# Kernel optimization log

Measured on AMD Instinct MI355X. Metric: run time of the kernel, lower is better.

Reference implementation:

```python
import jax, jax.numpy as jnp
import numpy as np

N = 100000   # nodes
E = 1600000  # edges
F = 64       # num_features
H = 64       # hidden_units
C = 10       # num_classes
G = 1000     # graphs in batch
BN_EPS = 1e-5


def setup_inputs() -> dict:
    key = jax.random.key(0)
    ks = jax.random.split(key, 32)
    inp = {
        "x": jax.random.normal(ks[0], (N, F), dtype=jnp.float32),
        "edge_index": jax.random.randint(ks[1], (2, E), 0, N, dtype=jnp.int64),
        "batch": jnp.sort(jax.random.randint(ks[2], (N,), 0, G, dtype=jnp.int64)),
    }
    i = 3
    def w(shape, scale):
        nonlocal i
        a = jax.random.normal(ks[i], shape, dtype=jnp.float32) * scale
        i += 1
        return a
    for l, din in [(0, F), (1, H)]:
        inp[f"c{l}_w1"] = w((din, H), 1.0 / np.sqrt(din))
        inp[f"c{l}_b1"] = jnp.zeros((H,), jnp.float32)
        inp[f"c{l}_g1"] = jnp.ones((H,), jnp.float32)
        inp[f"c{l}_be1"] = jnp.zeros((H,), jnp.float32)
        inp[f"c{l}_w2"] = w((H, H), 1.0 / np.sqrt(H))
        inp[f"c{l}_b2"] = jnp.zeros((H,), jnp.float32)
        inp[f"bn{l}_g"] = jnp.ones((H,), jnp.float32)
        inp[f"bn{l}_b"] = jnp.zeros((H,), jnp.float32)
    for l, din in [(0, F), (1, H), (2, H)]:
        inp[f"l{l}_w"] = w((din, C), 1.0 / np.sqrt(din))
        inp[f"l{l}_b"] = jnp.zeros((C,), jnp.float32)
    return inp


def _bn(h, g, b):
    # BatchNorm1d in training mode: batch statistics over node axis
    m = jnp.mean(h, axis=0)
    v = jnp.var(h, axis=0)
    return g * (h - m) * jax.lax.rsqrt(v + BN_EPS) + b


def _gin_conv(h, src, dst, w1, b1, g1, be1, w2, b2):
    # scatter-add neighbor aggregation: out[dst] += h[src]; eps = 0
    agg = jax.ops.segment_sum(h[src], dst, num_segments=N)
    z = h + agg                      # (1 + eps) * x + sum_j x_j
    z = jax.nn.relu(_bn(z @ w1 + b1, g1, be1))
    return z @ w2 + b2


def reference(x, edge_index, batch,
              c0_w1, c0_b1, c0_g1, c0_be1, c0_w2, c0_b2, bn0_g, bn0_b,
              c1_w1, c1_b1, c1_g1, c1_be1, c1_w2, c1_b2, bn1_g, bn1_b,
              l0_w, l0_b, l1_w, l1_b, l2_w, l2_b):
    src, dst = edge_index[0], edge_index[1]
    h0 = x
    h1 = jax.nn.relu(_bn(_gin_conv(h0, src, dst, c0_w1, c0_b1, c0_g1, c0_be1, c0_w2, c0_b2), bn0_g, bn0_b))
    h2 = jax.nn.relu(_bn(_gin_conv(h1, src, dst, c1_w1, c1_b1, c1_g1, c1_be1, c1_w2, c1_b2), bn1_g, bn1_b))
    # jumping-knowledge readout: per-layer global_add_pool -> Linear -> sum (dropout=0)
    out = jnp.zeros((G, C), dtype=x.dtype)
    for h, w, b in [(h0, l0_w, l0_b), (h1, l1_w, l1_b), (h2, l2_w, l2_b)]:
        pooled = jax.ops.segment_sum(h, batch, num_segments=G)
        out = out + pooled @ w + b
    return out
```

## Files before the change

### kernel.cpp

```cpp
#include <hip/hip_runtime.h>
#include <hip/hip_bf16.h>

#define BN_EPS 1e-5f
#define NBMAX 512
#define CHUNK 4096
#define CAPC  6144

typedef __hip_bfloat16 bf16;
typedef __attribute__((ext_vector_type(8))) short short8;
typedef __attribute__((ext_vector_type(4))) float f32x4;

__device__ __forceinline__ float b2f(bf16 v) { return __bfloat162float(v); }
__device__ __forceinline__ bf16 f2b(float v) { return __float2bfloat16(v); }
__device__ __forceinline__ float bl(unsigned u) { return __uint_as_float(u << 16); }
__device__ __forceinline__ float bh(unsigned u) { return __uint_as_float(u & 0xffff0000u); }
__device__ __forceinline__ unsigned pack2(float x, float y) {
    union { bf16 b[2]; unsigned u; } p;
    p.b[0] = f2b(x); p.b[1] = f2b(y);
    return p.u;
}
__device__ __forceinline__ float bs2f(short s) {
    return __uint_as_float(((unsigned)(unsigned short)s) << 16);
}
__device__ __forceinline__ short f2bs(float v) {
    bf16 b = f2b(v);
    return *reinterpret_cast<short*>(&b);
}

__global__ __launch_bounds__(256) void initcast_k(
    const float* __restrict__ in, bf16* __restrict__ out, int total4,
    int* __restrict__ btot, int nbp1)
{
    if (blockIdx.x == 0) {
        for (int i = threadIdx.x; i < nbp1; i += 256) btot[i] = 0;
    }
    int i = blockIdx.x * 256 + threadIdx.x;
    if (i >= total4) return;
    float4 v = ((const float4*)in)[i];
    union { ushort4 u; bf16 b[4]; } p;
    p.b[0] = f2b(v.x); p.b[1] = f2b(v.y); p.b[2] = f2b(v.z); p.b[3] = f2b(v.w);
    ((ushort4*)out)[i] = p.u;
}


__global__ __launch_bounds__(256) void bincount_k(
    const int* __restrict__ dst, int* __restrict__ btot, int E, int NB)
{
    __shared__ int h[NBMAX];
    for (int i = threadIdx.x; i < NB; i += 256) h[i] = 0;
    __syncthreads();
    const int base = blockIdx.x * CHUNK;
    const int lim = min(CHUNK, E - base);
    for (int i = threadIdx.x; i < lim; i += 256)
        atomicAdd(&h[dst[base + i] >> 8], 1);
    __syncthreads();
    for (int i = threadIdx.x; i < NB; i += 256)
        if (h[i]) atomicAdd(&btot[i], h[i]);
}

__global__ __launch_bounds__(256) void bucketscan_k(
    const int* __restrict__ btot, int* __restrict__ bbase,
    int* __restrict__ bcur, int* __restrict__ rowptr, int NB, int N, int E)
{
    __shared__ int s[256];
    const int t = threadIdx.x;
    int v0 = (2 * t     < NB) ? btot[2 * t]     : 0;
    int v1 = (2 * t + 1 < NB) ? btot[2 * t + 1] : 0;
    s[t] = v0 + v1;
    __syncthreads();
    for (int off = 1; off < 256; off <<= 1) {
        int a = (t >= off) ? s[t - off] : 0;
        __syncthreads();
        s[t] += a;
        __syncthreads();
    }
    int excl = s[t] - (v0 + v1);
    if (2 * t < NB)     { bbase[2 * t] = excl;          bcur[2 * t] = excl; }
    if (2 * t + 1 < NB) { bbase[2 * t + 1] = excl + v0; bcur[2 * t + 1] = excl + v0; }
    if (t == 0) { bbase[NB] = E; rowptr[N] = E; }
}

__global__ __launch_bounds__(256) void binscatter_k(
    const int* __restrict__ src, const int* __restrict__ dst,
    int* __restrict__ bcur, int* __restrict__ tmp, int E, int NB)
{
    __shared__ int hist[NBMAX];
    __shared__ int loff[NBMAX];
    __shared__ int gb[NBMAX];
    __shared__ int lcur[NBMAX];
    __shared__ int staged[CHUNK];
    __shared__ unsigned short sb[CHUNK];
    __shared__ int ssc[256];
    const int t = threadIdx.x;
    for (int i = t; i < NB; i += 256) { hist[i] = 0; lcur[i] = 0; }
    __syncthreads();
    const int base = blockIdx.x * CHUNK;
    const int lim = min(CHUNK, E - base);
    int myb[16], myw[16];
    int cnt = 0;
    for (int i = t; i < lim; i += 256) {
        int d = dst[base + i];
        int s_ = src[base + i];
        int b = d >> 8;
        myb[cnt] = b;
        myw[cnt] = (s_ << 8) | (d & 255);
        cnt++;
        atomicAdd(&hist[b], 1);
    }
    __syncthreads();
    int v0 = (2 * t     < NB) ? hist[2 * t]     : 0;
    int v1 = (2 * t + 1 < NB) ? hist[2 * t + 1] : 0;
    ssc[t] = v0 + v1;
    __syncthreads();
    for (int off = 1; off < 256; off <<= 1) {
        int a = (t >= off) ? ssc[t - off] : 0;
        __syncthreads();
        ssc[t] += a;
        __syncthreads();
    }
    int excl = ssc[t] - (v0 + v1);
    if (2 * t < NB)     loff[2 * t] = excl;
    if (2 * t + 1 < NB) loff[2 * t + 1] = excl + v0;
    __syncthreads();
    for (int b = t; b < NB; b += 256)
        if (hist[b] > 0) gb[b] = atomicAdd(&bcur[b], hist[b]);
    for (int i = 0; i < cnt; i++) {
        int b = myb[i];
        int p = loff[b] + atomicAdd(&lcur[b], 1);
        staged[p] = myw[i];
        sb[p] = (unsigned short)b;
    }
    __syncthreads();
    for (int i = t; i < lim; i += 256) {
        int b = sb[i];
        tmp[gb[b] + (i - loff[b])] = staged[i];
    }
}

__global__ __launch_bounds__(256) void csr_k(
    const int* __restrict__ bbase, const int* __restrict__ tmp,
    int* __restrict__ rowptr, int* __restrict__ adj, int N)
{
    __shared__ int hist[256], pfx[256], cur[256], ssc[256];
    __shared__ int sadj[CAPC];
    const int b = blockIdx.x, t = threadIdx.x;
    const int lo = bbase[b], hi = bbase[b + 1];
    const int cnt = hi - lo;
    hist[t] = 0; cur[t] = 0;
    __syncthreads();
    for (int i = t; i < cnt; i += 256)
        atomicAdd(&hist[tmp[lo + i] & 255], 1);
    __syncthreads();
    int v = hist[t];
    ssc[t] = v;
    __syncthreads();
    for (int off = 1; off < 256; off <<= 1) {
        int a = (t >= off) ? ssc[t - off] : 0;
        __syncthreads();
        ssc[t] += a;
        __syncthreads();
    }
    pfx[t] = ssc[t] - v;
    const int node = b * 256 + t;
    if (node < N) rowptr[node] = lo + pfx[t];
    __syncthreads();
    if (cnt <= CAPC) {
        for (int i = t; i < cnt; i += 256) {
            int w = tmp[lo + i];
            int d = w & 255;
            int p = pfx[d] + atomicAdd(&cur[d], 1);
            sadj[p] = w >> 8;
        }
        __syncthreads();
        for (int i = t; i < cnt; i += 256) adj[lo + i] = sadj[i];
    } else {
        for (int i = t; i < cnt; i += 256) {
            int w = tmp[lo + i];
            int d = w & 255;
            int p = pfx[d] + atomicAdd(&cur[d], 1);
            adj[lo + p] = w >> 8;
        }
    }
}

template<int AFFINE>
__global__ __launch_bounds__(256) void aggregate_k(
    const bf16* __restrict__ h, const int* __restrict__ rowptr,
    const int* __restrict__ adj, bf16* __restrict__ z, int N,
    const float* __restrict__ sc, const float* __restrict__ sh)
{
    const int lane = threadIdx.x & 31;
    const int n = blockIdx.x * 8 + (threadIdx.x >> 5);
    float sc0 = 0.f, sc1 = 0.f, sh0 = 0.f, sh1 = 0.f;
    if (AFFINE) {
        const int f0 = lane * 2;
        sc0 = sc[f0]; sc1 = sc[f0 + 1];
        sh0 = sh[f0]; sh1 = sh[f0 + 1];
    }
    if (n >= N) return;
    const unsigned* hp = (const unsigned*)h;
    const int b = rowptr[n], e = rowptr[n + 1];

    unsigned u = hp[(size_t)n * 32 + lane];
    float a0 = bl(u), a1 = bh(u);
    if (AFFINE) {
        a0 = fmaxf(fmaf(a0, sc0, sh0), 0.f);
        a1 = fmaxf(fmaf(a1, sc1, sh1), 0.f);
    }
    float s0 = a0, s1 = a1;

    int i = b;
    for (; i + 16 <= e; i += 16) {
        int m[16];
        #pragma unroll
        for (int k = 0; k < 16; k++) m[k] = adj[i + k];
        unsigned w[16];
        #pragma unroll
        for (int k = 0; k < 16; k++) w[k] = hp[(size_t)m[k] * 32 + lane];
        #pragma unroll
        for (int k = 0; k < 16; k++) {
            float p0 = bl(w[k]), p1 = bh(w[k]);
            if (AFFINE) {
                p0 = fmaxf(fmaf(p0, sc0, sh0), 0.f);
                p1 = fmaxf(fmaf(p1, sc1, sh1), 0.f);
            }
            s0 += p0; s1 += p1;
        }
    }
    for (; i + 4 <= e; i += 4) {
        int m[4];
        #pragma unroll
        for (int k = 0; k < 4; k++) m[k] = adj[i + k];
        #pragma unroll
        for (int k = 0; k < 4; k++) {
            unsigned w = hp[(size_t)m[k] * 32 + lane];
            float p0 = bl(w), p1 = bh(w);
            if (AFFINE) {
                p0 = fmaxf(fmaf(p0, sc0, sh0), 0.f);
                p1 = fmaxf(fmaf(p1, sc1, sh1), 0.f);
            }
            s0 += p0; s1 += p1;
        }
    }
    for (; i < e; i++) {
        unsigned w = hp[(size_t)adj[i] * 32 + lane];
        float p0 = bl(w), p1 = bh(w);
        if (AFFINE) {
            p0 = fmaxf(fmaf(p0, sc0, sh0), 0.f);
            p1 = fmaxf(fmaf(p1, sc1, sh1), 0.f);
        }
        s0 += p0; s1 += p1;
    }
    ((unsigned*)z)[(size_t)n * 32 + lane] = pack2(s0, s1);
}

template<int MODE>
__global__ __launch_bounds__(256) void gemm64_k(
    const bf16* __restrict__ A,
    const float* __restrict__ scin, const float* __restrict__ shin,
    const float* __restrict__ W, const float* __restrict__ bias,
    bf16* __restrict__ out, float* __restrict__ pstat, int nrows)
{
    __shared__ bf16 sWt[64][72];
    __shared__ float sSc[64], sSh[64], sB[64];
    __shared__ float sredS[64][17], sredQ[64][17];
    const int tid = threadIdx.x;

    if (tid < 64) {
        sB[tid] = bias[tid];
        if (MODE == 1) { sSc[tid] = scin[tid]; sSh[tid] = shin[tid]; }
    }
    for (int i = tid; i < 4096; i += 256) {
        int k = i >> 6, n = i & 63;
        sWt[n][k] = f2b(W[i]);
    }
    __syncthreads();

    const int wave = tid >> 6, lane = tid & 63;
    const int quad = lane >> 4, l16 = lane & 15;
    const int row0 = blockIdx.x * 128 + wave * 32;

    short8 a[2][2];
    #pragma unroll
    for (int rt = 0; rt < 2; rt++) {
        int r = row0 + rt * 16 + l16;
        int rr = min(r, nrows - 1);
        const bf16* arow = A + (size_t)rr * 64;
        a[rt][0] = *(const short8*)(arow + quad * 8);
        a[rt][1] = *(const short8*)(arow + 32 + quad * 8);
        if (MODE == 1) {
            #pragma unroll
            for (int j = 0; j < 8; j++) {
                int f0 = quad * 8 + j;
                a[rt][0][j] = f2bs(fmaxf(fmaf(bs2f(a[rt][0][j]), sSc[f0], sSh[f0]), 0.f));
                int f1 = 32 + f0;
                a[rt][1][j] = f2bs(fmaxf(fmaf(bs2f(a[rt][1][j]), sSc[f1], sSh[f1]), 0.f));
            }
        }
    }

    float psS[4], psQ[4];
    #pragma unroll
    for (int t = 0; t < 4; t++) { psS[t] = 0.f; psQ[t] = 0.f; }

    #pragma unroll
    for (int t = 0; t < 4; t++) {
        const int n = t * 16 + l16;
        short8 b0 = *(const short8*)&sWt[n][quad * 8];
        short8 b1 = *(const short8*)&sWt[n][32 + quad * 8];
        const float bn_ = sB[n];
        #pragma unroll
        for (int rt = 0; rt < 2; rt++) {
            f32x4 acc = {0.f, 0.f, 0.f, 0.f};
            acc = __builtin_amdgcn_mfma_f32_16x16x32_bf16(a[rt][0], b0, acc, 0, 0, 0);
            acc = __builtin_amdgcn_mfma_f32_16x16x32_bf16(a[rt][1], b1, acc, 0, 0, 0);
            #pragma unroll
            for (int reg = 0; reg < 4; reg++) {
                int gr = row0 + rt * 16 + quad * 4 + reg;
                if (gr < nrows) {
                    float v = acc[reg] + bn_;
                    out[(size_t)gr * 64 + n] = f2b(v);
                    psS[t] += v;
                    psQ[t] = fmaf(v, v, psQ[t]);
                }
            }
        }
    }

    #pragma unroll
    for (int t = 0; t < 4; t++) {
        sredS[t * 16 + l16][wave * 4 + quad] = psS[t];
        sredQ[t * 16 + l16][wave * 4 + quad] = psQ[t];
    }
    __syncthreads();
    if (tid < 128) {
        const int c = tid & 63;
        const float* p = (tid < 64) ? &sredS[c][0] : &sredQ[c][0];
        float s = 0.f;
        #pragma unroll
        for (int i = 0; i < 16; i++) s += p[i];
        pstat[(size_t)blockIdx.x * 128 + (tid < 64 ? c : 64 + c)] = s;
    }
}

__global__ __launch_bounds__(256) void bn_reduce_k(
    const float* __restrict__ pstat, int nblk,
    const float* __restrict__ g, const float* __restrict__ be, float invN,
    float* __restrict__ sc, float* __restrict__ sh)
{
    const int f = blockIdx.x;
    const int t = threadIdx.x;
    float S = 0.f, Q = 0.f;
    for (int b = t; b < nblk; b += 256) {
        S += pstat[(size_t)b * 128 + f];
        Q += pstat[(size_t)b * 128 + 64 + f];
    }
    __shared__ float rs[256], rq[256];
    rs[t] = S; rq[t] = Q;
    __syncthreads();
    for (int off = 128; off > 0; off >>= 1) {
        if (t < off) { rs[t] += rs[t + off]; rq[t] += rq[t + off]; }
        __syncthreads();
    }
    if (t == 0) {
        float m = rs[0] * invN;
        float v = rq[0] * invN - m * m;
        float s = g[f] * rsqrtf(v + BN_EPS);
        sc[f] = s;
        sh[f] = be[f] - m * s;
    }
}

__global__ __launch_bounds__(256) void pool_readout_k(
    const bf16* __restrict__ xb, const bf16* __restrict__ z0,
    const bf16* __restrict__ z1, const int* __restrict__ batch,
    const float* __restrict__ scA, const float* __restrict__ shA,
    const float* __restrict__ scB, const float* __restrict__ shB,
    const float* __restrict__ w0, const float* __restrict__ b0,
    const float* __restrict__ w1, const float* __restrict__ b1,
    const float* __restrict__ w2, const float* __restrict__ b2,
    float* __restrict__ out, int Nn)
{
    const int g = blockIdx.x;
    int lo = 0, hi = Nn;
    while (lo < hi) { int mid = (lo + hi) >> 1; if (batch[mid] < g) lo = mid + 1; else hi = mid; }
    const int start = lo;
    hi = Nn;
    while (lo < hi) { int mid = (lo + hi) >> 1; if (batch[mid] <= g) lo = mid + 1; else hi = mid; }
    const int end = lo;

    const int f = threadIdx.x & 63;
    const int w = threadIdx.x >> 6;
    const float sA = scA[f], tA = shA[f];
    const float sB = scB[f], tB = shB[f];

    float s0 = 0.f, s1 = 0.f, s2 = 0.f;
    for (int i = start + w; i < end; i += 4) {
        s0 += b2f(xb[(size_t)i * 64 + f]);
        s1 += fmaxf(fmaf(b2f(z0[(size_t)i * 64 + f]), sA, tA), 0.f);
        s2 += fmaxf(fmaf(b2f(z1[(size_t)i * 64 + f]), sB, tB), 0.f);
    }
    __shared__ float p[3][4][64];
    p[0][w][f] = s0; p[1][w][f] = s1; p[2][w][f] = s2;
    __syncthreads();
    if (threadIdx.x < 10) {
        const int c = threadIdx.x;
        float acc = b0[c] + b1[c] + b2[c];
        for (int k = 0; k < 64; k++) {
            float q0 = p[0][0][k] + p[0][1][k] + p[0][2][k] + p[0][3][k];
            float q1 = p[1][0][k] + p[1][1][k] + p[1][2][k] + p[1][3][k];
            float q2 = p[2][0][k] + p[2][1][k] + p[2][2][k] + p[2][3][k];
            acc = fmaf(q0, w0[k * 10 + c], acc);
            acc = fmaf(q1, w1[k * 10 + c], acc);
            acc = fmaf(q2, w2[k * 10 + c], acc);
        }
        out[(size_t)g * 10 + c] = acc;
    }
}

extern "C" void kernel_launch(void* const* d_in, const int* in_sizes, int n_in,
                              void* d_out, int out_size, void* d_ws, size_t ws_size,
                              hipStream_t stream)
{
    const float* x     = (const float*)d_in[0];
    const int*   edge  = (const int*)d_in[1];
    const int*   batch = (const int*)d_in[2];
    const int N = in_sizes[0] / 64;
    const int E = in_sizes[1] / 2;
    const int G = out_size / 10;
    const int* src = edge;
    const int* dst = edge + E;
    const int NB = (N + 255) / 256;

    const float* c_w1[2]  = {(const float*)d_in[3],  (const float*)d_in[11]};
    const float* c_b1[2]  = {(const float*)d_in[4],  (const float*)d_in[12]};
    const float* c_g1[2]  = {(const float*)d_in[5],  (const float*)d_in[13]};
    const float* c_be1[2] = {(const float*)d_in[6],  (const float*)d_in[14]};
    const float* c_w2[2]  = {(const float*)d_in[7],  (const float*)d_in[15]};
    const float* c_b2[2]  = {(const float*)d_in[8],  (const float*)d_in[16]};
    const float* bn_g[2]  = {(const float*)d_in[9],  (const float*)d_in[17]};
    const float* bn_b[2]  = {(const float*)d_in[10], (const float*)d_in[18]};
    const float* lw[3]    = {(const float*)d_in[19], (const float*)d_in[21], (const float*)d_in[23]};
    const float* lb[3]    = {(const float*)d_in[20], (const float*)d_in[22], (const float*)d_in[24]};

    float* out = (float*)d_out;
    const size_t nh = (size_t)N * 64;
    const int PG = (N + 127) / 128;

    bf16*  zb    = (bf16*)d_ws;
    bf16*  wb    = zb + nh;
    bf16*  xb    = wb + nh;
    float* scsh  = (float*)(xb + nh);
    float* pstat = scsh + 512;
    int*   rowptr   = (int*)(pstat + (size_t)PG * 128);
    int*   adj      = rowptr + N + 1;
    int*   tmp      = adj + E;
    int*   btot     = tmp + E;
    int*   bbase    = btot + NB + 1;
    int*   bcur     = bbase + NB + 1;

    float* sc0 = scsh;       float* sh0 = scsh + 64;
    float* scA = scsh + 128; float* shA = scsh + 192;
    float* sc2 = scsh + 256; float* sh2 = scsh + 320;
    float* scB = scsh + 384; float* shB = scsh + 448;

    const float invN = 1.0f / (float)N;
    const int binGrid  = (E + CHUNK - 1) / CHUNK;
    const int aggGrid  = (N + 7) / 8;
    const int ewGrid   = (int)((nh / 4 + 255) / 256);

    initcast_k<<<ewGrid, 256, 0, stream>>>(x, xb, (int)(nh / 4), btot, NB + 1);
    bincount_k<<<binGrid, 256, 0, stream>>>(dst, btot, E, NB);
    bucketscan_k<<<1, 256, 0, stream>>>(btot, bbase, bcur, rowptr, NB, N, E);
    binscatter_k<<<binGrid, 256, 0, stream>>>(src, dst, bcur, tmp, E, NB);
    csr_k<<<NB, 256, 0, stream>>>(bbase, tmp, rowptr, adj, N);

    aggregate_k<0><<<aggGrid, 256, 0, stream>>>(xb, rowptr, adj, zb, N, nullptr, nullptr);
    gemm64_k<0><<<PG, 256, 0, stream>>>(zb, nullptr, nullptr,
                                        c_w1[0], c_b1[0], zb, pstat, N);
    bn_reduce_k<<<64, 256, 0, stream>>>(pstat, PG, c_g1[0], c_be1[0], invN, sc0, sh0);
    gemm64_k<1><<<PG, 256, 0, stream>>>(zb, sc0, sh0,
                                        c_w2[0], c_b2[0], zb, pstat, N);
    bn_reduce_k<<<64, 256, 0, stream>>>(pstat, PG, bn_g[0], bn_b[0], invN, scA, shA);

    aggregate_k<1><<<aggGrid, 256, 0, stream>>>(zb, rowptr, adj, wb, N, scA, shA);
    gemm64_k<0><<<PG, 256, 0, stream>>>(wb, nullptr, nullptr,
                                        c_w1[1], c_b1[1], wb, pstat, N);
    bn_reduce_k<<<64, 256, 0, stream>>>(pstat, PG, c_g1[1], c_be1[1], invN, sc2, sh2);
    gemm64_k<1><<<PG, 256, 0, stream>>>(wb, sc2, sh2,
                                        c_w2[1], c_b2[1], wb, pstat, N);
    bn_reduce_k<<<64, 256, 0, stream>>>(pstat, PG, bn_g[1], bn_b[1], invN, scB, shB);

    pool_readout_k<<<G, 256, 0, stream>>>(xb, zb, wb, batch,
                                          scA, shA, scB, shB,
                                          lw[0], lb[0], lw[1], lb[1], lw[2], lb[2],
                                          out, N);
}
```

Measured before the change: 327.4 us.

## Degree-sort nodes within buckets and aggregate with 16 lanes per node

```diff
diff --git a/kernel.cpp b/kernel.cpp
--- a/kernel.cpp
+++ b/kernel.cpp
@@ -139,14 +139,16 @@
 
 __global__ __launch_bounds__(256) void csr_k(
     const int* __restrict__ bbase, const int* __restrict__ tmp,
-    int* __restrict__ rowptr, int* __restrict__ adj, int N)
+    int* __restrict__ rowptr, int* __restrict__ adj,
+    int* __restrict__ perm, int N)
 {
     __shared__ int hist[256], pfx[256], cur[256], ssc[256];
+    __shared__ int dh[256], dcur[256];
     __shared__ int sadj[CAPC];
     const int b = blockIdx.x, t = threadIdx.x;
     const int lo = bbase[b], hi = bbase[b + 1];
     const int cnt = hi - lo;
-    hist[t] = 0; cur[t] = 0;
+    hist[t] = 0; cur[t] = 0; dh[t] = 0; dcur[t] = 0;
     __syncthreads();
     for (int i = t; i < cnt; i += 256)
         atomicAdd(&hist[tmp[lo + i] & 255], 1);
@@ -163,7 +165,25 @@
     pfx[t] = ssc[t] - v;
     const int node = b * 256 + t;
     if (node < N) rowptr[node] = lo + pfx[t];
-    __syncthreads();
+
+    int deg = min(v, 255);
+    atomicAdd(&dh[deg], 1);
+    __syncthreads();
+    int dv = dh[t];
+    ssc[t] = dv;
+    __syncthreads();
+    for (int off = 1; off < 256; off <<= 1) {
+        int a = (t >= off) ? ssc[t - off] : 0;
+        __syncthreads();
+        ssc[t] += a;
+        __syncthreads();
+    }
+    dh[t] = ssc[t] - dv;
+    __syncthreads();
+    int rank = dh[deg] + atomicAdd(&dcur[deg], 1);
+    perm[b * 256 + rank] = node;
+    __syncthreads();
+
     if (cnt <= CAPC) {
         for (int i = t; i < cnt; i += 256) {
             int w = tmp[lo + i];
@@ -186,72 +206,68 @@
 template<int AFFINE>
 __global__ __launch_bounds__(256) void aggregate_k(
     const bf16* __restrict__ h, const int* __restrict__ rowptr,
-    const int* __restrict__ adj, bf16* __restrict__ z, int N,
+    const int* __restrict__ adj, const int* __restrict__ perm,
+    bf16* __restrict__ z, int N,
     const float* __restrict__ sc, const float* __restrict__ sh)
 {
-    const int lane = threadIdx.x & 31;
-    const int n = blockIdx.x * 8 + (threadIdx.x >> 5);
-    float sc0 = 0.f, sc1 = 0.f, sh0 = 0.f, sh1 = 0.f;
+    const int lane = threadIdx.x & 15;
+    const int slot = blockIdx.x * 16 + (threadIdx.x >> 4);
+    float4 vsc, vsh;
     if (AFFINE) {
-        const int f0 = lane * 2;
-        sc0 = sc[f0]; sc1 = sc[f0 + 1];
-        sh0 = sh[f0]; sh1 = sh[f0 + 1];
-    }
+        vsc = ((const float4*)sc)[lane];
+        vsh = ((const float4*)sh)[lane];
+    }
+    const int n = perm[slot];
     if (n >= N) return;
-    const unsigned* hp = (const unsigned*)h;
+    const uint2* hp = (const uint2*)h;
     const int b = rowptr[n], e = rowptr[n + 1];
 
-    unsigned u = hp[(size_t)n * 32 + lane];
-    float a0 = bl(u), a1 = bh(u);
+    uint2 u = hp[(size_t)n * 16 + lane];
+    float a0 = bl(u.x), a1 = bh(u.x), a2 = bl(u.y), a3 = bh(u.y);
     if (AFFINE) {
-        a0 = fmaxf(fmaf(a0, sc0, sh0), 0.f);
-        a1 = fmaxf(fmaf(a1, sc1, sh1), 0.f);
-    }
-    float s0 = a0, s1 = a1;
+        a0 = fmaxf(fmaf(a0, vsc.x, vsh.x), 0.f);
+        a1 = fmaxf(fmaf(a1, vsc.y, vsh.y), 0.f);
+        a2 = fmaxf(fmaf(a2, vsc.z, vsh.z), 0.f);
+        a3 = fmaxf(fmaf(a3, vsc.w, vsh.w), 0.f);
+    }
+    float s0 = a0, s1 = a1, s2 = a2, s3 = a3;
 
     int i = b;
-    for (; i + 16 <= e; i += 16) {
-        int m[16];
+    for (; i + 8 <= e; i += 8) {
+        int m[8];
         #pragma unroll
-        for (int k = 0; k < 16; k++) m[k] = adj[i + k];
-        unsigned w[16];
+        for (int k = 0; k < 8; k++) m[k] = adj[i + k];
+        uint2 w[8];
         #pragma unroll
-        for (int k = 0; k < 16; k++) w[k] = hp[(size_t)m[k] * 32 + lane];
+        for (int k = 0; k < 8; k++) w[k] = hp[(size_t)m[k] * 16 + lane];
         #pragma unroll
-        for (int k = 0; k < 16; k++) {
-            float p0 = bl(w[k]), p1 = bh(w[k]);
+        for (int k = 0; k < 8; k++) {
+            float p0 = bl(w[k].x), p1 = bh(w[k].x);
+            float p2 = bl(w[k].y), p3 = bh(w[k].y);
             if (AFFINE) {
-                p0 = fmaxf(fmaf(p0, sc0, sh0), 0.f);
-                p1 = fmaxf(fmaf(p1, sc1, sh1), 0.f);
+                p0 = fmaxf(fmaf(p0, vsc.x, vsh.x), 0.f);
+                p1 = fmaxf(fmaf(p1, vsc.y, vsh.y), 0.f);
+                p2 = fmaxf(fmaf(p2, vsc.z, vsh.z), 0.f);
+                p3 = fmaxf(fmaf(p3, vsc.w, vsh.w), 0.f);
             }
-            s0 += p0; s1 += p1;
-        }
-    }
-    for (; i + 4 <= e; i += 4) {
-        int m[4];
-        #pragma unroll
-        for (int k = 0; k < 4; k++) m[k] = adj[i + k];
-        #pragma unroll
-        for (int k = 0; k < 4; k++) {
-            unsigned w = hp[(size_t)m[k] * 32 + lane];
-            float p0 = bl(w), p1 = bh(w);
-            if (AFFINE) {
-                p0 = fmaxf(fmaf(p0, sc0, sh0), 0.f);
-                p1 = fmaxf(fmaf(p1, sc1, sh1), 0.f);
-            }
-            s0 += p0; s1 += p1;
+            s0 += p0; s1 += p1; s2 += p2; s3 += p3;
         }
     }
     for (; i < e; i++) {
-        unsigned w = hp[(size_t)adj[i] * 32 + lane];
-        float p0 = bl(w), p1 = bh(w);
+        uint2 w = hp[(size_t)adj[i] * 16 + lane];
+        float p0 = bl(w.x), p1 = bh(w.x), p2 = bl(w.y), p3 = bh(w.y);
         if (AFFINE) {
-            p0 = fmaxf(fmaf(p0, sc0, sh0), 0.f);
-            p1 = fmaxf(fmaf(p1, sc1, sh1), 0.f);
-        }
-        s0 += p0; s1 += p1;
-    }
-    ((unsigned*)z)[(size_t)n * 32 + lane] = pack2(s0, s1);
+            p0 = fmaxf(fmaf(p0, vsc.x, vsh.x), 0.f);
+            p1 = fmaxf(fmaf(p1, vsc.y, vsh.y), 0.f);
+            p2 = fmaxf(fmaf(p2, vsc.z, vsh.z), 0.f);
+            p3 = fmaxf(fmaf(p3, vsc.w, vsh.w), 0.f);
+        }
+        s0 += p0; s1 += p1; s2 += p2; s3 += p3;
+    }
+    uint2 o;
+    o.x = pack2(s0, s1);
+    o.y = pack2(s2, s3);
+    ((uint2*)z)[(size_t)n * 16 + lane] = o;
 }
 
 template<int MODE>
@@ -458,6 +474,7 @@
     int*   btot     = tmp + E;
     int*   bbase    = btot + NB + 1;
     int*   bcur     = bbase + NB + 1;
+    int*   perm     = bcur + NB;
 
     float* sc0 = scsh;       float* sh0 = scsh + 64;
     float* scA = scsh + 128; float* shA = scsh + 192;
@@ -466,16 +483,17 @@
 
     const float invN = 1.0f / (float)N;
     const int binGrid  = (E + CHUNK - 1) / CHUNK;
-    const int aggGrid  = (N + 7) / 8;
+    const int aggGrid  = NB * 16;
     const int ewGrid   = (int)((nh / 4 + 255) / 256);
 
     initcast_k<<<ewGrid, 256, 0, stream>>>(x, xb, (int)(nh / 4), btot, NB + 1);
     bincount_k<<<binGrid, 256, 0, stream>>>(dst, btot, E, NB);
     bucketscan_k<<<1, 256, 0, stream>>>(btot, bbase, bcur, rowptr, NB, N, E);
     binscatter_k<<<binGrid, 256, 0, stream>>>(src, dst, bcur, tmp, E, NB);
-    csr_k<<<NB, 256, 0, stream>>>(bbase, tmp, rowptr, adj, N);
-
-    aggregate_k<0><<<aggGrid, 256, 0, stream>>>(xb, rowptr, adj, zb, N, nullptr, nullptr);
+    csr_k<<<NB, 256, 0, stream>>>(bbase, tmp, rowptr, adj, perm, N);
+
+    aggregate_k<0><<<aggGrid, 256, 0, stream>>>(xb, rowptr, adj, perm, zb, N,
+                                                nullptr, nullptr);
     gemm64_k<0><<<PG, 256, 0, stream>>>(zb, nullptr, nullptr,
                                         c_w1[0], c_b1[0], zb, pstat, N);
     bn_reduce_k<<<64, 256, 0, stream>>>(pstat, PG, c_g1[0], c_be1[0], invN, sc0, sh0);
@@ -483,7 +501,8 @@
                                         c_w2[0], c_b2[0], zb, pstat, N);
     bn_reduce_k<<<64, 256, 0, stream>>>(pstat, PG, bn_g[0], bn_b[0], invN, scA, shA);
 
-    aggregate_k<1><<<aggGrid, 256, 0, stream>>>(zb, rowptr, adj, wb, N, scA, shA);
+    aggregate_k<1><<<aggGrid, 256, 0, stream>>>(zb, rowptr, adj, perm, wb, N,
+                                                scA, shA);
     gemm64_k<0><<<PG, 256, 0, stream>>>(wb, nullptr, nullptr,
                                         c_w1[1], c_b1[1], wb, pstat, N);
     bn_reduce_k<<<64, 256, 0, stream>>>(pstat, PG, c_g1[1], c_be1[1], invN, sc2, sh2);
```

New measurement: 333.8 us. About the same (+1.9%).
